# Kernel tuning notes

Hardware: AMD Instinct MI355X
Metric: run time of the kernel (lower is better)

The kernel has to match this reference:

```python
import jax, jax.numpy as jnp
import numpy as np

B, T, D_MODEL, H, W = 2, 3, 32, 256, 256
N_HEADS, N_LEVELS, N_POINTS = 4, 3, 4


def conv2d(x, w, b, padding=1, dilation=1):
    y = jax.lax.conv_general_dilated(
        x, w, window_strides=(1, 1),
        padding=[(padding, padding), (padding, padding)],
        rhs_dilation=(dilation, dilation),
        dimension_numbers=('NCHW', 'OIHW', 'NCHW'))
    return y + b[None, :, None, None]


def lrelu(x):
    return jnp.where(x >= 0, x, 0.1 * x)


def bilinear_sample(img, x, y):
    # img: (N,C,H,W); x,y: (N,H',W') pixel coords; zero padding outside (grid_sample zeros)
    N, C, Hh, Ww = img.shape
    x0 = jnp.floor(x); y0 = jnp.floor(y)
    lx = x - x0; ly = y - y0
    imf = img.reshape(N, C, Hh * Ww)
    out = jnp.zeros((N, C) + x.shape[1:], img.dtype)
    for dy, dx, wgt in ((0, 0, (1 - lx) * (1 - ly)), (0, 1, lx * (1 - ly)),
                        (1, 0, (1 - lx) * ly), (1, 1, lx * ly)):
        xi = x0 + dx; yi = y0 + dy
        valid = (xi >= 0) & (xi < Ww) & (yi >= 0) & (yi < Hh)
        idx = (jnp.clip(yi, 0, Hh - 1) * Ww + jnp.clip(xi, 0, Ww - 1)).astype(jnp.int32)
        g = jnp.take_along_axis(imf, idx.reshape(N, 1, -1), axis=2).reshape((N, C) + x.shape[1:])
        out = out + g * (wgt * valid)[:, None]
    return out


def flow_warp(x, flow):
    # torch flow_warp with align_corners=True == sampling at pixel coords grid+flow
    N, C, Hh, Ww = x.shape
    gy, gx = jnp.meshgrid(jnp.arange(Hh, dtype=x.dtype), jnp.arange(Ww, dtype=x.dtype), indexing='ij')
    return bilinear_sample(x, gx[None] + flow[:, 0], gy[None] + flow[:, 1])


def ms_deform_attn(value, sampling_locations, attention_weights, h, w):
    # value: (N, L*h*w, Hh, d); loc: (N, Lq, Hh, L, P, 2) in [0,1]; weights: (N, Lq, Hh, L, P)
    # Matches MSDA CUDA kernel: sample at loc*(W,H)-0.5, bilinear, zero pad outside.
    N, _, Hh, d = value.shape
    Lq = sampling_locations.shape[1]
    L, P = sampling_locations.shape[3], sampling_locations.shape[4]
    out = jnp.zeros((N, Lq, Hh, d), value.dtype)
    for l in range(L):
        v = value[:, l * h * w:(l + 1) * h * w].transpose(0, 2, 1, 3)  # (N,Hh,hw,d)
        loc = sampling_locations[:, :, :, l]  # (N,Lq,Hh,P,2)
        x = loc[..., 0] * w - 0.5
        y = loc[..., 1] * h - 0.5
        x0 = jnp.floor(x); y0 = jnp.floor(y)
        lx = x - x0; ly = y - y0
        samp = jnp.zeros((N, Lq, Hh, P, d), value.dtype)
        for dy, dx, wgt in ((0, 0, (1 - lx) * (1 - ly)), (0, 1, lx * (1 - ly)),
                            (1, 0, (1 - lx) * ly), (1, 1, lx * ly)):
            xi = x0 + dx; yi = y0 + dy
            valid = (xi >= 0) & (xi < w) & (yi >= 0) & (yi < h)
            idx = (jnp.clip(yi, 0, h - 1) * w + jnp.clip(xi, 0, w - 1)).astype(jnp.int32)
            idx = idx.transpose(0, 2, 1, 3).reshape(N, Hh, Lq * P)
            g = jnp.take_along_axis(v, idx[..., None], axis=2)  # (N,Hh,Lq*P,d)
            g = g.reshape(N, Hh, Lq, P, d).transpose(0, 2, 1, 3, 4)
            samp = samp + g * (wgt * valid)[..., None]
        out = out + (samp * attention_weights[:, :, :, l][..., None]).sum(axis=3)
    return out.reshape(N, Lq, Hh * d)


def setup_inputs() -> dict:
    key = jax.random.key(0)
    ks = jax.random.split(key, 24)
    def rn(k, shape, s=1.0):
        return jax.random.normal(k, shape, dtype=jnp.float32) * s
    c = D_MODEL
    nofp = N_HEADS * N_LEVELS * N_POINTS
    return {
        'frame': rn(ks[0], (B, T, c, H, W)),
        'srcframe': rn(ks[1], (B, T, c, H, W)),
        'flow_forward': rn(ks[2], (B, T - 1, 2, H, W), 2.0),
        'flow_backward': rn(ks[3], (B, T - 1, 2, H, W), 2.0),
        'W_qk': rn(ks[4], (3 * c, 3 * c + 4, 3, 3), 0.05), 'b_qk': rn(ks[5], (3 * c,), 0.05),
        'W_v': rn(ks[6], (3 * c, 3 * c, 3, 3), 0.05), 'b_v': rn(ks[7], (3 * c,), 0.05),
        'W_vp': rn(ks[8], (c, c, 3, 3), 0.05), 'b_vp': rn(ks[9], (c,), 0.05),
        'W_off': rn(ks[10], (nofp * 2, 3 * c, 3, 3), 0.01), 'b_off': rn(ks[11], (nofp * 2,), 0.5),
        'W_aw': rn(ks[12], (nofp, 3 * c, 3, 3), 0.05), 'b_aw': rn(ks[13], (nofp,), 0.05),
        'W_out': rn(ks[14], (c, c, 3, 3), 0.05), 'b_out': rn(ks[15], (c,), 0.05),
        'W_ffd': rn(ks[16], (c, c, 3, 3), 0.05), 'b_ffd': rn(ks[17], (c,), 0.05),
        'W_ff1': rn(ks[18], (c, 2 * c, 3, 3), 0.05), 'b_ff1': rn(ks[19], (c,), 0.05),
        'W_ff2': rn(ks[20], (c, c, 3, 3), 0.05), 'b_ff2': rn(ks[21], (c,), 0.05),
        'W_fu': rn(ks[22], (c, c, 1, 1), 0.05), 'b_fu': rn(ks[23], (c,), 0.05),
    }


def reference(frame, srcframe, flow_forward, flow_backward,
              W_qk, b_qk, W_v, b_v, W_vp, b_vp, W_off, b_off, W_aw, b_aw,
              W_out, b_out, W_ffd, b_ffd, W_ff1, b_ff1, W_ff2, b_ff2, W_fu, b_fu):
    b, t, c, h, w = frame.shape
    Hh, L, P = N_HEADS, N_LEVELS, N_POINTS
    d = c // Hh
    # flow-warped neighbor frames + flows -> query embedding
    warp01 = flow_warp(frame[:, 0], flow_backward[:, 0])
    warp21 = flow_warp(frame[:, 2], flow_forward[:, 1])
    qk_in = jnp.concatenate([warp01, frame[:, 1], warp21,
                             flow_forward[:, 1], flow_backward[:, 0]], axis=1)
    qureys = lrelu(conv2d(qk_in, W_qk, b_qk))                       # (b, 3c, h, w)
    value = conv2d(frame.reshape(b, t * c, h, w), W_v, b_v)         # (b, 3c, h, w)
    # --- MSDeformAttn_Fusion ---
    val = conv2d(value.reshape(b * t, c, h, w), W_vp, b_vp).reshape(b, t, c, h, w)
    off = conv2d(qureys, W_off, b_off)                               # (b, Hh*L*P*2, h, w)
    aw = conv2d(qureys, W_aw, b_aw)                                  # (b, Hh*L*P, h, w)
    value_flat = val.reshape(b, t, c, h * w).transpose(0, 1, 3, 2).reshape(b, t * h * w, Hh, d)
    off = off.reshape(b, -1, h * w).transpose(0, 2, 1).reshape(b, h * w, Hh, L, P, 2)
    aw = aw.reshape(b, -1, h * w).transpose(0, 2, 1).reshape(b, h * w, Hh, L * P)
    aw = jax.nn.softmax(aw, axis=-1).reshape(b, h * w, Hh, L, P)
    # reference points: pixel centers normalized (masks all zero -> valid_ratios == 1)
    gy, gx = jnp.meshgrid((jnp.arange(h, dtype=off.dtype) + 0.5) / h,
                          (jnp.arange(w, dtype=off.dtype) + 0.5) / w, indexing='ij')
    ref = jnp.stack([gx.reshape(-1), gy.reshape(-1)], -1)            # (hw, 2) (x, y)
    normalizer = jnp.array([w, h], dtype=off.dtype)                  # same for all levels
    loc = ref[None, :, None, None, None, :] + off / normalizer
    attn_out = ms_deform_attn(value_flat, loc, aw, h, w)             # (b, hw, c)
    out = attn_out.reshape(b, h, w, c).transpose(0, 3, 1, 2)
    out = conv2d(out, W_out, b_out)                                  # output_proj
    # --- post-attention ---
    out = conv2d(out, W_ffd, b_ffd) + frame[:, 1]
    tseq = jnp.concatenate([out, srcframe[:, 1]], axis=1)            # (b, 2c, h, w)
    ff = conv2d(lrelu(conv2d(tseq, W_ff1, b_ff1, padding=2, dilation=2)), W_ff2, b_ff2)
    out = out + ff
    out = lrelu(conv2d(out, W_fu, b_fu, padding=0))                  # fusion 1x1
    return out
```

## Files before the change

### kernel.cpp

```cpp
#include <hip/hip_runtime.h>
#include <hip/hip_bf16.h>

typedef __hip_bfloat16 bf16;
typedef unsigned short us;
typedef __attribute__((ext_vector_type(8))) short short8;
typedef __attribute__((ext_vector_type(8))) unsigned short ushortx8;
typedef __attribute__((ext_vector_type(4))) float f32x4;

#define HW 65536
#define IMW 256
#define IMH 256

static __device__ __forceinline__ float u2f(us u) {
  return __uint_as_float(((unsigned)u) << 16);
}
static __device__ __forceinline__ us f2bu(float x) {
  bf16 h = __float2bfloat16(x);
  return *reinterpret_cast<us*>(&h);
}
static __device__ __forceinline__ unsigned pk2(float a, float b) {
  return (unsigned)f2bu(a) | ((unsigned)f2bu(b) << 16);
}

struct PrepArgs {
  const float* src[9];
  us* dst[9];
  int OC[9], CIN[9], KPAD[9];
};

__global__ __launch_bounds__(256) void prep_weights(PrepArgs a) {
  int j = blockIdx.y;
  int n = blockIdx.x * 256 + threadIdx.x;
  int OC = a.OC[j], CIN = a.CIN[j], KPAD = a.KPAD[j];
  int tot = 9 * OC * KPAD;
  if (n >= tot) return;
  int G = OC >> 4, NKC = KPAD >> 5;
  int e = n & 7;
  int m = (n >> 3) & 15;
  int q = (n >> 7) & 3;
  int rest = n >> 9;
  int kc = rest % NKC;
  int tg = rest / NKC;
  int g = tg % G;
  int t = tg / G;
  int oc = g * 16 + m;
  int k = kc * 32 + q * 8 + e;
  float v = (k < CIN) ? a.src[j][(size_t)(oc * CIN + k) * 9 + t] : 0.f;
  a.dst[j][n] = f2bu(v);
}

__global__ __launch_bounds__(256) void frame_to_nhwc(const float* __restrict__ frame,
                                                     unsigned* __restrict__ fn) {
  int pix = blockIdx.x * 256 + threadIdx.x;
  int b = blockIdx.y;
  const float* s = frame + (size_t)b * 96 * HW + pix;
  unsigned u[48];
#pragma unroll
  for (int j = 0; j < 48; ++j)
    u[j] = pk2(s[(size_t)(2 * j) * HW], s[(size_t)(2 * j + 1) * HW]);
  unsigned* d = fn + ((size_t)b * HW + pix) * 48;
#pragma unroll
  for (int j = 0; j < 12; ++j) {
    uint4 w;
    w.x = u[4 * j]; w.y = u[4 * j + 1]; w.z = u[4 * j + 2]; w.w = u[4 * j + 3];
    *(uint4*)&d[4 * j] = w;
  }
}

static __device__ void warp_nhwc(const us* __restrict__ fn, size_t bbase, int coff,
                                 float x, float y, unsigned* uo) {
  float x0f = floorf(x), y0f = floorf(y);
  float lx = x - x0f, ly = y - y0f;
  int x0 = (int)x0f, y0 = (int)y0f;
  float wt[4] = {(1.f - lx) * (1.f - ly), lx * (1.f - ly), (1.f - lx) * ly, lx * ly};
  float acc[32] = {};
#pragma unroll
  for (int k = 0; k < 4; ++k) {
    int xi = x0 + (k & 1), yi = y0 + (k >> 1);
    if ((unsigned)xi < IMW && (unsigned)yi < IMH) {
      const ushortx8* s =
          (const ushortx8*)(fn + (bbase + (size_t)yi * IMW + xi) * 96 + coff);
      float w = wt[k];
#pragma unroll
      for (int cj = 0; cj < 4; ++cj) {
        ushortx8 vv = s[cj];
#pragma unroll
        for (int e = 0; e < 8; ++e)
          acc[cj * 8 + e] = fmaf(w, u2f(vv[e]), acc[cj * 8 + e]);
      }
    }
  }
#pragma unroll
  for (int j = 0; j < 16; ++j) uo[j] = pk2(acc[2 * j], acc[2 * j + 1]);
}

__global__ __launch_bounds__(256) void build_qkin(
    const us* __restrict__ fn, const float* __restrict__ flowf,
    const float* __restrict__ flowb, unsigned* __restrict__ qk) {
  int pix = blockIdx.x * 256 + threadIdx.x;
  int b = blockIdx.y;
  int px = pix & 255, py = pix >> 8;

  float fbx = flowb[((size_t)(b * 2 + 0) * 2 + 0) * HW + pix];
  float fby = flowb[((size_t)(b * 2 + 0) * 2 + 1) * HW + pix];
  float ffx = flowf[((size_t)(b * 2 + 1) * 2 + 0) * HW + pix];
  float ffy = flowf[((size_t)(b * 2 + 1) * 2 + 1) * HW + pix];

  unsigned u[50];
  {
    const unsigned* s = (const unsigned*)(fn + ((size_t)b * HW + pix) * 96);
#pragma unroll
    for (int j = 0; j < 16; ++j) u[16 + j] = s[16 + j];
  }
  u[48] = pk2(ffx, ffy);
  u[49] = pk2(fbx, fby);

  warp_nhwc(fn, (size_t)b * HW, 0, (float)px + fbx, (float)py + fby, &u[0]);
  warp_nhwc(fn, (size_t)b * HW, 64, (float)px + ffx, (float)py + ffy, &u[32]);

  unsigned* qb = qk + ((size_t)b * HW + pix) * 50;
#pragma unroll
  for (int j = 0; j < 25; ++j) {
    uint2 t;
    t.x = u[2 * j];
    t.y = u[2 * j + 1];
    *(uint2*)(qb + 2 * j) = t;
  }
}

template <int CIN, int CST, int KPAD, int DIL, int G, int ZDIV, int CSUB,
          int RES, int OUTMODE, bool LRELU>
__global__ __launch_bounds__(256) void conv3x3_mfma(
    const us* __restrict__ in, const us* __restrict__ W2,
    const float* __restrict__ bias, void* __restrict__ out, int out_cst,
    int out_coff, float* __restrict__ outB, const float* __restrict__ res,
    int res_cst, int res_coff) {
  constexpr int OC = G * 16;
  constexpr int COLS = 16 + 2 * DIL;
  constexpr int ROWS = 8 + 2 * DIL;
  constexpr int HALO = ROWS * COLS;
  constexpr int CIPAD = KPAD + 8;
  constexpr int CH = KPAD / 8;
  constexpr int NKC = KPAD / 32;
  constexpr int GW0 = (G + 1) / 2;
  constexpr int NU = 9 * NKC;
  __shared__ alignas(16) short lds[HALO * CIPAD];

  const int z = blockIdx.z;
  const int bin = z / ZDIV;
  const int coff = (z % ZDIV) * CSUB;
  const int px0 = blockIdx.x * 16, py0 = blockIdx.y * 8;
  const int lane = threadIdx.x & 63;
  const int wv = threadIdx.x >> 6;
  const int m = lane & 15, q = lane >> 4;
  const int gh = wv & 1, rh = wv >> 1;
  const int goff = gh * GW0;

  f32x4 acc[GW0][4];
#pragma unroll
  for (int g = 0; g < GW0; ++g)
#pragma unroll
    for (int r = 0; r < 4; ++r) acc[g][r] = 0.f;

  for (int c = threadIdx.x; c < HALO * CH; c += 256) {
    int p = c / CH, cb = c - p * CH;
    int row = p / COLS, col = p - row * COLS;
    int gy = py0 + row - DIL, gx = px0 + col - DIL;
    bool ok = ((unsigned)gy < IMH) && ((unsigned)gx < IMW);
    int ci0 = cb * 8;
    const us* gp = in + ((size_t)bin * HW + (size_t)gy * IMW + gx) * CST + coff + ci0;
    if (CIN == KPAD) {
      short8 v = (short8)0;
      if (ok) v = *(const short8*)gp;
      *(short8*)&lds[p * CIPAD + ci0] = v;
    } else {
      uint2 h0; h0.x = 0; h0.y = 0;
      uint2 h1; h1.x = 0; h1.y = 0;
      if (ok && ci0 + 4 <= CIN) h0 = *(const uint2*)gp;
      if (ok && ci0 + 8 <= CIN) h1 = *(const uint2*)(gp + 4);
      *(uint2*)&lds[p * CIPAD + ci0] = h0;
      *(uint2*)&lds[p * CIPAD + ci0 + 4] = h1;
    }
  }
  __syncthreads();

  const us* wl = W2 + (size_t)lane * 8;
  short8 af[2][GW0];
#pragma unroll
  for (int g = 0; g < GW0; ++g)
    if (goff + g < G)
      af[0][g] = *(const short8*)(wl + (size_t)((goff + g) * NKC) * 512);

#pragma unroll
  for (int u = 0; u < NU; ++u) {
    const int t = u / NKC, kc = u - t * NKC;
    if (u + 1 < NU) {
      const int t1 = (u + 1) / NKC, kc1 = (u + 1) - t1 * NKC;
#pragma unroll
      for (int g = 0; g < GW0; ++g)
        if (goff + g < G)
          af[(u + 1) & 1][g] =
              *(const short8*)(wl + (size_t)((t1 * G + goff + g) * NKC + kc1) * 512);
    }
    const int dy = t / 3 - 1, dx = t - (t / 3) * 3 - 1;
    short8 bfr[4];
#pragma unroll
    for (int r = 0; r < 4; ++r) {
      int rr = rh * 4 + r + DIL + dy * DIL;
      int cc = m + DIL + dx * DIL;
      bfr[r] = *(const short8*)&lds[(rr * COLS + cc) * CIPAD + kc * 32 + q * 8];
    }
#pragma unroll
    for (int g = 0; g < GW0; ++g)
      if (goff + g < G)
#pragma unroll
        for (int r = 0; r < 4; ++r)
          acc[g][r] = __builtin_amdgcn_mfma_f32_16x16x32_bf16(af[u & 1][g], bfr[r],
                                                              acc[g][r], 0, 0, 0);
  }

#pragma unroll
  for (int g = 0; g < GW0; ++g) {
    if (goff + g < G) {
      int oc0 = (goff + g) * 16 + q * 4;
      f32x4 bb = *(const f32x4*)&bias[oc0];
#pragma unroll
      for (int r = 0; r < 4; ++r) {
        int py = py0 + rh * 4 + r;
        int px = px0 + m;
        size_t pix = (size_t)py * IMW + px;
        f32x4 v;
#pragma unroll
        for (int e = 0; e < 4; ++e) {
          float x = acc[g][r][e] + bb[e];
          if (LRELU) x = x >= 0.f ? x : 0.1f * x;
          v[e] = x;
        }
        if (RES == 1) {
          f32x4 rv = *(const f32x4*)&res[((size_t)z * HW + pix) * res_cst + oc0];
#pragma unroll
          for (int e = 0; e < 4; ++e) v[e] += rv[e];
        }
        if (RES == 2) {
#pragma unroll
          for (int e = 0; e < 4; ++e)
            v[e] += res[((size_t)z * res_cst + res_coff + oc0 + e) * HW + pix];
        }
        if (OUTMODE == 0 || OUTMODE == 3) {
          uint2 w;
          w.x = pk2(v[0], v[1]);
          w.y = pk2(v[2], v[3]);
          *(uint2*)&((us*)out)[((size_t)z * HW + pix) * out_cst + out_coff + oc0] = w;
        }
        if (OUTMODE == 2)
          *(f32x4*)&((float*)out)[((size_t)z * HW + pix) * out_cst + oc0] = v;
        if (OUTMODE == 3)
          *(f32x4*)&outB[((size_t)z * HW + pix) * 32 + oc0] = v;
      }
    }
  }
}

__global__ __launch_bounds__(256) void deform_attn(
    const us* __restrict__ valp, const us* __restrict__ off,
    const float* __restrict__ aw, us* __restrict__ outp) {
  int tid = threadIdx.x;
  int hh = tid & 3;
  int pix = blockIdx.x * 64 + (tid >> 2);
  int b = blockIdx.y;
  int px = pix & (IMW - 1), py = pix >> 8;
  float refx = ((float)px + 0.5f) * (1.0f / IMW);
  float refy = ((float)py + 0.5f) * (1.0f / IMH);

  ushortx8 o8[3];
  {
    const ushortx8* ob =
        (const ushortx8*)(off + ((size_t)b * HW + pix) * 96 + hh * 24);
#pragma unroll
    for (int j = 0; j < 3; ++j) o8[j] = ob[j];
  }
  f32x4 a4[3];
  {
    const f32x4* ab = (const f32x4*)(aw + ((size_t)b * HW + pix) * 48 + hh * 12);
#pragma unroll
    for (int j = 0; j < 3; ++j) a4[j] = ab[j];
  }

  float wv[12];
  float mx = -1e30f;
#pragma unroll
  for (int lp = 0; lp < 12; ++lp) {
    wv[lp] = a4[lp >> 2][lp & 3];
    mx = fmaxf(mx, wv[lp]);
  }
  float s = 0.f;
#pragma unroll
  for (int lp = 0; lp < 12; ++lp) {
    wv[lp] = __expf(wv[lp] - mx);
    s += wv[lp];
  }
  float inv = 1.f / s;

  float acc[8] = {0.f, 0.f, 0.f, 0.f, 0.f, 0.f, 0.f, 0.f};
#pragma unroll 1
  for (int l = 0; l < 3; ++l) {
    const us* vbase = valp + ((size_t)(b * 3 + l) * HW) * 32 + hh * 8;
#pragma unroll
    for (int p = 0; p < 4; ++p) {
      int ch = l * 8 + p * 2;
      float ox = u2f(o8[ch >> 3][ch & 7]);
      float oy = u2f(o8[(ch + 1) >> 3][(ch + 1) & 7]);
      float x = (refx + ox * (1.0f / IMW)) * (float)IMW - 0.5f;
      float y = (refy + oy * (1.0f / IMH)) * (float)IMH - 0.5f;
      float x0f = floorf(x), y0f = floorf(y);
      float lx = x - x0f, ly = y - y0f;
      int x0 = (int)x0f, y0 = (int)y0f;
      float a = wv[l * 4 + p] * inv;
      float cw[4] = {(1.f - lx) * (1.f - ly) * a, lx * (1.f - ly) * a,
                     (1.f - lx) * ly * a, lx * ly * a};
#pragma unroll
      for (int k = 0; k < 4; ++k) {
        int xi = x0 + (k & 1), yi = y0 + (k >> 1);
        if ((unsigned)xi < IMW && (unsigned)yi < IMH) {
          const ushortx8 u = *(const ushortx8*)(vbase + (size_t)(yi * IMW + xi) * 32);
          float wgt = cw[k];
#pragma unroll
          for (int dd = 0; dd < 8; ++dd) acc[dd] = fmaf(wgt, u2f(u[dd]), acc[dd]);
        }
      }
    }
  }
  ushortx8 sv;
#pragma unroll
  for (int dd = 0; dd < 8; ++dd) sv[dd] = f2bu(acc[dd]);
  *(ushortx8*)(outp + ((size_t)b * HW + pix) * 32 + hh * 8) = sv;
}

__global__ __launch_bounds__(256) void copy_src(const float* __restrict__ src,
                                                unsigned* __restrict__ out1b) {
  int pix = blockIdx.x * 256 + threadIdx.x;
  int b = blockIdx.y;
  const float* s = src + ((size_t)(b * 3 + 1) * 32) * HW + pix;
  unsigned u[16];
#pragma unroll
  for (int j = 0; j < 16; ++j)
    u[j] = pk2(s[(size_t)(2 * j) * HW], s[(size_t)(2 * j + 1) * HW]);
  unsigned* d = out1b + ((size_t)b * HW + pix) * 32 + 16;
#pragma unroll
  for (int j = 0; j < 4; ++j) {
    uint4 w;
    w.x = u[4 * j]; w.y = u[4 * j + 1]; w.z = u[4 * j + 2]; w.w = u[4 * j + 3];
    *(uint4*)&d[4 * j] = w;
  }
}

__global__ __launch_bounds__(256) void conv1x1_fu(
    const float* __restrict__ in, const float* __restrict__ wgt,
    const float* __restrict__ bias, float* __restrict__ out) {
  int pix = blockIdx.x * 256 + threadIdx.x;
  int b = blockIdx.y;
  float vin[32];
  {
    const f32x4* s = (const f32x4*)(in + ((size_t)b * HW + pix) * 32);
#pragma unroll
    for (int j = 0; j < 8; ++j) {
      f32x4 v = s[j];
#pragma unroll
      for (int e = 0; e < 4; ++e) vin[4 * j + e] = v[e];
    }
  }
#pragma unroll 1
  for (int oc = 0; oc < 32; ++oc) {
    float a = bias[oc];
#pragma unroll
    for (int ci = 0; ci < 32; ++ci) a = fmaf(wgt[oc * 32 + ci], vin[ci], a);
    a = a >= 0.f ? a : 0.1f * a;
    out[((size_t)b * 32 + oc) * HW + pix] = a;
  }
}

extern "C" void kernel_launch(void* const* d_in, const int* in_sizes, int n_in,
                              void* d_out, int out_size, void* d_ws, size_t ws_size,
                              hipStream_t stream) {
  (void)in_sizes; (void)n_in; (void)out_size;
  if (ws_size < 25614592ull * 4) return;

  const float* frame = (const float*)d_in[0];
  const float* srcframe = (const float*)d_in[1];
  const float* flowf = (const float*)d_in[2];
  const float* flowb = (const float*)d_in[3];

  float* ws = (float*)d_ws;
  us* wsu = (us*)d_ws;

  static const int w2off[9] = {0,      110592, 193536, 202752, 285696,
                               327168, 336384, 345600, 364032};
  us* fnhwc = (us*)(ws + 186624);
  unsigned* qk_u = (unsigned*)(ws + 6478080);
  us* qk = (us*)qk_u;
  us* Q = (us*)(ws + 13031680);
  us* V = (us*)(ws + 6478080);
  us* Vp = (us*)(ws + 19323136);
  us* offb = (us*)(ws + 186624);
  float* awb = (float*)(ws + 6478080);
  us* attn = (us*)(ws + 13031680);
  us* convout = (us*)(ws + 13031680 + 2097152);
  us* out1b = (us*)(ws + 6478080);
  unsigned* out1b_u = (unsigned*)out1b;
  float* out1f = (float*)(ws + 19323136);
  us* ff1out = (us*)(ws + 186624);
  float* out2 = (float*)(ws + 13031680);

  {
    PrepArgs pa;
    static const int srcidx[9] = {4, 6, 8, 10, 12, 14, 16, 18, 20};
    static const int OCs[9] = {96, 96, 32, 96, 48, 32, 32, 32, 32};
    static const int CINs[9] = {100, 96, 32, 96, 96, 32, 32, 64, 32};
    static const int KPADs[9] = {128, 96, 32, 96, 96, 32, 32, 64, 32};
    for (int i = 0; i < 9; ++i) {
      pa.src[i] = (const float*)d_in[srcidx[i]];
      pa.dst[i] = wsu + w2off[i];
      pa.OC[i] = OCs[i];
      pa.CIN[i] = CINs[i];
      pa.KPAD[i] = KPADs[i];
    }
    prep_weights<<<dim3(432, 9), 256, 0, stream>>>(pa);
  }

  frame_to_nhwc<<<dim3(256, 2), 256, 0, stream>>>(frame, (unsigned*)fnhwc);

  build_qkin<<<dim3(256, 2), 256, 0, stream>>>(fnhwc, flowf, flowb, qk_u);

  dim3 cg2(16, 32, 2);

  conv3x3_mfma<100, 100, 128, 1, 6, 1, 0, 0, 0, true><<<cg2, 256, 0, stream>>>(
      qk, wsu + w2off[0], (const float*)d_in[5], Q, 96, 0, nullptr, nullptr, 0, 0);

  conv3x3_mfma<96, 96, 96, 1, 6, 1, 0, 0, 0, false><<<cg2, 256, 0, stream>>>(
      fnhwc, wsu + w2off[1], (const float*)d_in[7], V, 96, 0, nullptr, nullptr, 0, 0);

  conv3x3_mfma<32, 96, 32, 1, 2, 3, 32, 0, 0, false><<<dim3(16, 32, 6), 256, 0, stream>>>(
      V, wsu + w2off[2], (const float*)d_in[9], Vp, 32, 0, nullptr, nullptr, 0, 0);

  conv3x3_mfma<96, 96, 96, 1, 6, 1, 0, 0, 0, false><<<cg2, 256, 0, stream>>>(
      Q, wsu + w2off[3], (const float*)d_in[11], offb, 96, 0, nullptr, nullptr, 0, 0);

  conv3x3_mfma<96, 96, 96, 1, 3, 1, 0, 0, 2, false><<<cg2, 256, 0, stream>>>(
      Q, wsu + w2off[4], (const float*)d_in[13], awb, 48, 0, nullptr, nullptr, 0, 0);

  deform_attn<<<dim3(1024, 2), 256, 0, stream>>>(Vp, offb, awb, attn);

  conv3x3_mfma<32, 32, 32, 1, 2, 1, 0, 0, 0, false><<<cg2, 256, 0, stream>>>(
      attn, wsu + w2off[5], (const float*)d_in[15], convout, 32, 0, nullptr, nullptr, 0, 0);

  conv3x3_mfma<32, 32, 32, 1, 2, 1, 0, 2, 3, false><<<cg2, 256, 0, stream>>>(
      convout, wsu + w2off[6], (const float*)d_in[17], out1b, 64, 0, out1f, frame, 96, 32);

  copy_src<<<dim3(256, 2), 256, 0, stream>>>(srcframe, out1b_u);

  conv3x3_mfma<64, 64, 64, 2, 2, 1, 0, 0, 0, true><<<cg2, 256, 0, stream>>>(
      out1b, wsu + w2off[7], (const float*)d_in[19], ff1out, 32, 0, nullptr, nullptr, 0, 0);

  conv3x3_mfma<32, 32, 32, 1, 2, 1, 0, 1, 2, false><<<cg2, 256, 0, stream>>>(
      ff1out, wsu + w2off[8], (const float*)d_in[21], out2, 32, 0, nullptr, out1f, 32, 0);

  conv1x1_fu<<<dim3(256, 2), 256, 0, stream>>>(out2, (const float*)d_in[22],
                                               (const float*)d_in[23], (float*)d_out);
}
```

Before: 481.8 us.

## Stage conv weights into double-buffered LDS via global_load_lds

Conv weight fragments are no longer loaded from global memory straight into registers. The block now copies each K-step's weight slice into a double-buffered LDS region using direct global-to-LDS loads, and waves read their MFMA A-fragments from LDS. The weight prep kernel is reordered so the g index is innermost within each (tap, kc) slice, making each step's slice contiguous. In exchange, the main loop gets a block-wide barrier every iteration and is no longer unrolled, which can serialize waves and reduce overlap.

```diff
diff --git a/kernel.cpp b/kernel.cpp
--- a/kernel.cpp
+++ b/kernel.cpp
@@ -3,6 +3,7 @@
 
 typedef __hip_bfloat16 bf16;
 typedef unsigned short us;
+typedef unsigned int u32;
 typedef __attribute__((ext_vector_type(8))) short short8;
 typedef __attribute__((ext_vector_type(8))) unsigned short ushortx8;
 typedef __attribute__((ext_vector_type(4))) float f32x4;
@@ -20,6 +21,12 @@
 }
 static __device__ __forceinline__ unsigned pk2(float a, float b) {
   return (unsigned)f2bu(a) | ((unsigned)f2bu(b) << 16);
+}
+
+static __device__ __forceinline__ void gload_lds16(const void* g, void* l) {
+  __builtin_amdgcn_global_load_lds(
+      (const __attribute__((address_space(1))) u32*)g,
+      (__attribute__((address_space(3))) u32*)l, 16, 0, 0);
 }
 
 struct PrepArgs {
@@ -36,13 +43,13 @@
   if (n >= tot) return;
   int G = OC >> 4, NKC = KPAD >> 5;
   int e = n & 7;
-  int m = (n >> 3) & 15;
-  int q = (n >> 7) & 3;
+  int q = (n >> 3) & 3;
+  int m = (n >> 5) & 15;
   int rest = n >> 9;
-  int kc = rest % NKC;
-  int tg = rest / NKC;
-  int g = tg % G;
-  int t = tg / G;
+  int g = rest % G;
+  int tkc = rest / G;
+  int kc = tkc % NKC;
+  int t = tkc / NKC;
   int oc = g * 16 + m;
   int k = kc * 32 + q * 8 + e;
   float v = (k < CIN) ? a.src[j][(size_t)(oc * CIN + k) * 9 + t] : 0.f;
@@ -144,7 +151,9 @@
   constexpr int NKC = KPAD / 32;
   constexpr int GW0 = (G + 1) / 2;
   constexpr int NU = 9 * NKC;
+  constexpr int WSLOT = G * 64;
   __shared__ alignas(16) short lds[HALO * CIPAD];
+  __shared__ alignas(16) short wlds[2][WSLOT * 8];
 
   const int z = blockIdx.z;
   const int bin = z / ZDIV;
@@ -182,27 +191,32 @@
       *(uint2*)&lds[p * CIPAD + ci0 + 4] = h1;
     }
   }
+
+#pragma unroll
+  for (int r = 0; r < (G + 3) / 4; ++r) {
+    int blk = r * 4 + wv;
+    if (blk * 64 < WSLOT)
+      gload_lds16(W2 + (size_t)(blk * 64 + lane) * 8, &wlds[0][blk * 64 * 8]);
+  }
   __syncthreads();
 
-  const us* wl = W2 + (size_t)lane * 8;
-  short8 af[2][GW0];
-#pragma unroll
-  for (int g = 0; g < GW0; ++g)
-    if (goff + g < G)
-      af[0][g] = *(const short8*)(wl + (size_t)((goff + g) * NKC) * 512);
-
-#pragma unroll
+  int buf = 0;
+#pragma unroll 1
   for (int u = 0; u < NU; ++u) {
+    if (u + 1 < NU) {
+      const us* wn = W2 + (size_t)(u + 1) * (WSLOT * 8);
+#pragma unroll
+      for (int r = 0; r < (G + 3) / 4; ++r) {
+        int blk = r * 4 + wv;
+        if (blk * 64 < WSLOT)
+          gload_lds16(wn + (size_t)(blk * 64 + lane) * 8,
+                      &wlds[buf ^ 1][blk * 64 * 8]);
+      }
+    }
+
     const int t = u / NKC, kc = u - t * NKC;
-    if (u + 1 < NU) {
-      const int t1 = (u + 1) / NKC, kc1 = (u + 1) - t1 * NKC;
-#pragma unroll
-      for (int g = 0; g < GW0; ++g)
-        if (goff + g < G)
-          af[(u + 1) & 1][g] =
-              *(const short8*)(wl + (size_t)((t1 * G + goff + g) * NKC + kc1) * 512);
-    }
     const int dy = t / 3 - 1, dx = t - (t / 3) * 3 - 1;
+
     short8 bfr[4];
 #pragma unroll
     for (int r = 0; r < 4; ++r) {
@@ -210,13 +224,21 @@
       int cc = m + DIL + dx * DIL;
       bfr[r] = *(const short8*)&lds[(rr * COLS + cc) * CIPAD + kc * 32 + q * 8];
     }
+    short8 af[GW0];
 #pragma unroll
     for (int g = 0; g < GW0; ++g)
       if (goff + g < G)
+        af[g] = *(const short8*)&wlds[buf][(((goff + g) * 16 + m) * 4 + q) * 8];
+
+#pragma unroll
+    for (int g = 0; g < GW0; ++g)
+      if (goff + g < G)
 #pragma unroll
         for (int r = 0; r < 4; ++r)
-          acc[g][r] = __builtin_amdgcn_mfma_f32_16x16x32_bf16(af[u & 1][g], bfr[r],
+          acc[g][r] = __builtin_amdgcn_mfma_f32_16x16x32_bf16(af[g], bfr[r],
                                                               acc[g][r], 0, 0, 0);
+    __syncthreads();
+    buf ^= 1;
   }
 
 #pragma unroll
```

New measurement: 511.3 us. +6.1%, slower.

## Add 32x32x16 MFMA conv kernel with async double-buffered weight staging

Applied to the files above, without the earlier changes.

Adds a new 3x3 conv kernel that computes with 32x32x16 bf16 MFMA instructions instead of the 16-wide tiles. Weights are streamed through double-buffered LDS using direct global-to-LDS loads, and prep_weights gains a matching weight layout. The three 96-output-channel convs (Q, V, offsets) are switched over to it. The aim is fewer MFMA and LDS operations per output and overlap of weight fetches with compute. The cost is more accumulator registers and a per-stage barrier.

```diff
diff --git a/kernel.cpp b/kernel.cpp
--- a/kernel.cpp
+++ b/kernel.cpp
@@ -3,9 +3,11 @@
 
 typedef __hip_bfloat16 bf16;
 typedef unsigned short us;
+typedef unsigned int u32;
 typedef __attribute__((ext_vector_type(8))) short short8;
 typedef __attribute__((ext_vector_type(8))) unsigned short ushortx8;
 typedef __attribute__((ext_vector_type(4))) float f32x4;
+typedef __attribute__((ext_vector_type(16))) float f32x16;
 
 #define HW 65536
 #define IMW 256
@@ -22,10 +24,16 @@
   return (unsigned)f2bu(a) | ((unsigned)f2bu(b) << 16);
 }
 
+static __device__ __forceinline__ void gload_lds16(const void* g, void* l) {
+  __builtin_amdgcn_global_load_lds(
+      (const __attribute__((address_space(1))) u32*)g,
+      (__attribute__((address_space(3))) u32*)l, 16, 0, 0);
+}
+
 struct PrepArgs {
   const float* src[9];
   us* dst[9];
-  int OC[9], CIN[9], KPAD[9];
+  int OC[9], CIN[9], KPAD[9], LAY[9];
 };
 
 __global__ __launch_bounds__(256) void prep_weights(PrepArgs a) {
@@ -34,19 +42,35 @@
   int OC = a.OC[j], CIN = a.CIN[j], KPAD = a.KPAD[j];
   int tot = 9 * OC * KPAD;
   if (n >= tot) return;
-  int G = OC >> 4, NKC = KPAD >> 5;
-  int e = n & 7;
-  int m = (n >> 3) & 15;
-  int q = (n >> 7) & 3;
-  int rest = n >> 9;
-  int kc = rest % NKC;
-  int tg = rest / NKC;
-  int g = tg % G;
-  int t = tg / G;
-  int oc = g * 16 + m;
-  int k = kc * 32 + q * 8 + e;
-  float v = (k < CIN) ? a.src[j][(size_t)(oc * CIN + k) * 9 + t] : 0.f;
-  a.dst[j][n] = f2bu(v);
+  int oc, k;
+  if (a.LAY[j] == 0) {
+    int G = OC >> 4, NKC = KPAD >> 5;
+    int e = n & 7;
+    int m = (n >> 3) & 15;
+    int q = (n >> 7) & 3;
+    int rest = n >> 9;
+    int kc = rest % NKC;
+    int tg = rest / NKC;
+    int g = tg % G;
+    int t = tg / G;
+    oc = g * 16 + m;
+    k = kc * 32 + q * 8 + e;
+    float v = (k < CIN) ? a.src[j][(size_t)(oc * CIN + k) * 9 + t] : 0.f;
+    a.dst[j][n] = f2bu(v);
+  } else {
+    int OCT = OC >> 5, KH = KPAD >> 4;
+    int e = n & 7;
+    int l = (n >> 3) & 63;
+    int rest = n >> 9;
+    int jt = rest % OCT;
+    int u = rest / OCT;
+    int kh = u % KH;
+    int t = u / KH;
+    oc = jt * 32 + (l & 31);
+    k = kh * 16 + (l >> 5) * 8 + e;
+    float v = (k < CIN) ? a.src[j][(size_t)(oc * CIN + k) * 9 + t] : 0.f;
+    a.dst[j][n] = f2bu(v);
+  }
 }
 
 __global__ __launch_bounds__(256) void frame_to_nhwc(const float* __restrict__ frame,
@@ -125,6 +149,126 @@
     t.x = u[2 * j];
     t.y = u[2 * j + 1];
     *(uint2*)(qb + 2 * j) = t;
+  }
+}
+
+template <int CIN, int CST, int KPAD, int OCT, int KHC, bool LRELU>
+__global__ __launch_bounds__(256) void conv3x3_m32(
+    const us* __restrict__ in, const us* __restrict__ W2,
+    const float* __restrict__ bias, us* __restrict__ out, int out_cst,
+    int out_coff) {
+  constexpr int COLS = 18, ROWS = 10, HALO = COLS * ROWS;
+  constexpr int CIPAD = KPAD + 8;
+  constexpr int CH = KPAD / 8;
+  constexpr int KH = KPAD / 16;
+  constexpr int SPT = KH / KHC;
+  constexpr int NSTG = 9 * SPT;
+  constexpr int CHB = KHC * OCT;
+  __shared__ alignas(16) short lds[HALO * CIPAD];
+  __shared__ alignas(16) short wlds[2][CHB * 512];
+
+  const int z = blockIdx.z;
+  const int px0 = blockIdx.x * 16, py0 = blockIdx.y * 8;
+  const int lane = threadIdx.x & 63;
+  const int wv = threadIdx.x >> 6;
+  const int n = lane & 31;
+  const int sr = n >> 4;
+  const int colp = n & 15;
+  const int kq = lane >> 5;
+
+  f32x16 acc[OCT];
+#pragma unroll
+  for (int j = 0; j < OCT; ++j) acc[j] = 0.f;
+
+  for (int c = threadIdx.x; c < HALO * CH; c += 256) {
+    int p = c / CH, cb = c - p * CH;
+    int row = p / COLS, col = p - row * COLS;
+    int gy = py0 + row - 1, gx = px0 + col - 1;
+    bool ok = ((unsigned)gy < IMH) && ((unsigned)gx < IMW);
+    int ci0 = cb * 8;
+    const us* gp = in + ((size_t)z * HW + (size_t)gy * IMW + gx) * CST + ci0;
+    if (CIN == KPAD) {
+      short8 v = (short8)0;
+      if (ok) v = *(const short8*)gp;
+      *(short8*)&lds[p * CIPAD + ci0] = v;
+    } else {
+      uint2 h0; h0.x = 0; h0.y = 0;
+      uint2 h1; h1.x = 0; h1.y = 0;
+      if (ok && ci0 + 4 <= CIN) h0 = *(const uint2*)gp;
+      if (ok && ci0 + 8 <= CIN) h1 = *(const uint2*)(gp + 4);
+      *(uint2*)&lds[p * CIPAD + ci0] = h0;
+      *(uint2*)&lds[p * CIPAD + ci0 + 4] = h1;
+    }
+  }
+
+#pragma unroll
+  for (int r = 0; r < (CHB + 3) / 4; ++r) {
+    int blk = r * 4 + wv;
+    if (blk < CHB)
+      gload_lds16(W2 + (size_t)(blk * 64 + lane) * 8, &wlds[0][blk * 512]);
+  }
+  __syncthreads();
+
+  const int lanebase = ((wv * 2 + sr) * COLS + colp) * CIPAD + kq * 8;
+
+  int buf = 0;
+#pragma unroll 1
+  for (int s = 0; s < NSTG; ++s) {
+    if (s + 1 < NSTG) {
+      const us* wn = W2 + (size_t)(s + 1) * (CHB * 512);
+#pragma unroll
+      for (int r = 0; r < (CHB + 3) / 4; ++r) {
+        int blk = r * 4 + wv;
+        if (blk < CHB)
+          gload_lds16(wn + (size_t)(blk * 64 + lane) * 8,
+                      &wlds[buf ^ 1][blk * 512]);
+      }
+    }
+    const int t = s / SPT;
+    const int kh0 = (s - t * SPT) * KHC;
+    const int dy = t / 3 - 1, dx = t - (t / 3) * 3 - 1;
+    const int sb = lanebase + ((dy + 1) * COLS + (dx + 1)) * CIPAD + kh0 * 16;
+#pragma unroll
+    for (int khr = 0; khr < KHC; ++khr) {
+      short8 bf = *(const short8*)&lds[sb + khr * 16];
+#pragma unroll
+      for (int j = 0; j < OCT; ++j) {
+        short8 af =
+            *(const short8*)&wlds[buf][(khr * OCT + j) * 512 + lane * 8];
+        acc[j] =
+            __builtin_amdgcn_mfma_f32_32x32x16_bf16(af, bf, acc[j], 0, 0, 0);
+      }
+    }
+    __syncthreads();
+    buf ^= 1;
+  }
+
+  {
+    int row = py0 + wv * 2 + sr;
+    int pxc = px0 + colp;
+    us* ob = out + ((size_t)z * HW + (size_t)row * IMW + pxc) * out_cst + out_coff;
+#pragma unroll
+    for (int j = 0; j < OCT; ++j) {
+#pragma unroll
+      for (int hi = 0; hi < 4; ++hi) {
+        int oc0 = j * 32 + hi * 8 + kq * 4;
+        f32x4 bb = *(const f32x4*)&bias[oc0];
+        float v0 = acc[j][4 * hi + 0] + bb[0];
+        float v1 = acc[j][4 * hi + 1] + bb[1];
+        float v2 = acc[j][4 * hi + 2] + bb[2];
+        float v3 = acc[j][4 * hi + 3] + bb[3];
+        if (LRELU) {
+          v0 = v0 >= 0.f ? v0 : 0.1f * v0;
+          v1 = v1 >= 0.f ? v1 : 0.1f * v1;
+          v2 = v2 >= 0.f ? v2 : 0.1f * v2;
+          v3 = v3 >= 0.f ? v3 : 0.1f * v3;
+        }
+        uint2 w;
+        w.x = pk2(v0, v1);
+        w.y = pk2(v2, v3);
+        *(uint2*)&ob[oc0] = w;
+      }
+    }
   }
 }
 
@@ -417,12 +561,14 @@
     static const int OCs[9] = {96, 96, 32, 96, 48, 32, 32, 32, 32};
     static const int CINs[9] = {100, 96, 32, 96, 96, 32, 32, 64, 32};
     static const int KPADs[9] = {128, 96, 32, 96, 96, 32, 32, 64, 32};
+    static const int LAYs[9] = {1, 1, 0, 1, 0, 0, 0, 0, 0};
     for (int i = 0; i < 9; ++i) {
       pa.src[i] = (const float*)d_in[srcidx[i]];
       pa.dst[i] = wsu + w2off[i];
       pa.OC[i] = OCs[i];
       pa.CIN[i] = CINs[i];
       pa.KPAD[i] = KPADs[i];
+      pa.LAY[i] = LAYs[i];
     }
     prep_weights<<<dim3(432, 9), 256, 0, stream>>>(pa);
   }
@@ -433,17 +579,17 @@
 
   dim3 cg2(16, 32, 2);
 
-  conv3x3_mfma<100, 100, 128, 1, 6, 1, 0, 0, 0, true><<<cg2, 256, 0, stream>>>(
-      qk, wsu + w2off[0], (const float*)d_in[5], Q, 96, 0, nullptr, nullptr, 0, 0);
-
-  conv3x3_mfma<96, 96, 96, 1, 6, 1, 0, 0, 0, false><<<cg2, 256, 0, stream>>>(
-      fnhwc, wsu + w2off[1], (const float*)d_in[7], V, 96, 0, nullptr, nullptr, 0, 0);
+  conv3x3_m32<100, 100, 128, 3, 4, true><<<cg2, 256, 0, stream>>>(
+      qk, wsu + w2off[0], (const float*)d_in[5], Q, 96, 0);
+
+  conv3x3_m32<96, 96, 96, 3, 6, false><<<cg2, 256, 0, stream>>>(
+      fnhwc, wsu + w2off[1], (const float*)d_in[7], V, 96, 0);
 
   conv3x3_mfma<32, 96, 32, 1, 2, 3, 32, 0, 0, false><<<dim3(16, 32, 6), 256, 0, stream>>>(
       V, wsu + w2off[2], (const float*)d_in[9], Vp, 32, 0, nullptr, nullptr, 0, 0);
 
-  conv3x3_mfma<96, 96, 96, 1, 6, 1, 0, 0, 0, false><<<cg2, 256, 0, stream>>>(
-      Q, wsu + w2off[3], (const float*)d_in[11], offb, 96, 0, nullptr, nullptr, 0, 0);
+  conv3x3_m32<96, 96, 96, 3, 6, false><<<cg2, 256, 0, stream>>>(
+      Q, wsu + w2off[3], (const float*)d_in[11], offb, 96, 0);
 
   conv3x3_mfma<96, 96, 96, 1, 3, 1, 0, 0, 2, false><<<cg2, 256, 0, stream>>>(
       Q, wsu + w2off[4], (const float*)d_in[13], awb, 48, 0, nullptr, nullptr, 0, 0);
```

Measured after the change: 465.0 us. 1.04x faster.
